# Performance work log

Hardware: AMD Instinct MI355X
Metric: run time of the kernel (lower is better)

The kernel has to match this reference:

```python
import jax, jax.numpy as jnp
import numpy as np

K = 10
EPS = 1e-5  # BatchNorm eps, eval mode with running_mean=0, running_var=1


def mish(x):
    return x * jnp.tanh(jax.nn.softplus(x))


def knn_idx(x, k):
    # x: (B, C, N); returns (B, N, k) indices of k nearest neighbors (incl. self)
    xx = jnp.sum(x * x, axis=1)                      # (B, N)
    inner = jnp.einsum('bcn,bcm->bnm', x, x)         # (B, N, N)
    neg_d = 2.0 * inner - xx[:, :, None] - xx[:, None, :]
    return jax.lax.top_k(neg_d, k)[1]


def graph_feature(x, k):
    # x: (B, C, N) -> edge features (B, 2C, N, k): cat(nbr - x, x)
    idx = knn_idx(x, k)
    x_t = jnp.transpose(x, (0, 2, 1))                # (B, N, C)
    nbr = jax.vmap(lambda xt, ix: xt[ix])(x_t, idx)  # (B, N, k, C)
    ctr = jnp.broadcast_to(x_t[:, :, None, :], nbr.shape)
    edge = jnp.concatenate([nbr - ctr, ctr], axis=-1)
    return jnp.transpose(edge, (0, 3, 1, 2))


def block2d(x, W, g, b):
    # Conv2d(kernel=1, bias=False) + BatchNorm2d(eval) + Mish
    y = jnp.einsum('oi,bink->bonk', W, x)
    y = y * (g / jnp.sqrt(1.0 + EPS))[None, :, None, None] + b[None, :, None, None]
    return mish(y)


def block1d(x, W, g, b):
    # Conv1d(kernel=1, bias=False) + BatchNorm1d(eval) + Mish
    y = jnp.einsum('oi,bin->bon', W, x)
    y = y * (g / jnp.sqrt(1.0 + EPS))[None, :, None] + b[None, :, None]
    return mish(y)


def setup_inputs() -> dict:
    key = jax.random.key(0)
    ks = jax.random.split(key, 32)
    B, N = 8, 4096
    x = jax.random.normal(ks[0], (B, 3, N), dtype=jnp.float32)

    def w(k, o, i):
        return jax.random.normal(k, (o, i), dtype=jnp.float32) * np.float32(np.sqrt(2.0 / i))

    W1 = w(ks[1], 64, 6)
    W2 = w(ks[2], 64, 128)
    W3 = w(ks[3], 128, 128)
    W4 = w(ks[4], 128, 128)
    W5 = w(ks[5], 128, 256)
    W6 = w(ks[6], 64, 128)
    W7 = w(ks[7], 64, 128)
    W8 = w(ks[8], 64, 128)
    W9 = w(ks[9], 2, 64)

    bn_sizes = [64, 64, 128, 128, 128, 64, 64, 64]
    gs, bs = [], []
    for i, c in enumerate(bn_sizes):
        gs.append(1.0 + 0.1 * jax.random.normal(ks[10 + i], (c,), dtype=jnp.float32))
        bs.append(0.1 * jax.random.normal(ks[20 + i], (c,), dtype=jnp.float32))

    d = {'x': x, 'W1': W1, 'W2': W2, 'W3': W3, 'W4': W4, 'W5': W5,
         'W6': W6, 'W7': W7, 'W8': W8, 'W9': W9}
    for i in range(8):
        d['g%d' % (i + 1)] = gs[i]
        d['b%d' % (i + 1)] = bs[i]
    return d


def reference(x, W1, W2, W3, W4, W5, W6, W7, W8, W9,
              g1, g2, g3, g4, g5, g6, g7, g8,
              b1, b2, b3, b4, b5, b6, b7, b8):
    e = graph_feature(x, K)                      # (B, 6, N, k)
    x1 = jnp.max(block2d(e, W1, g1, b1), axis=-1)  # (B, 64, N)
    e = graph_feature(x1, K)                     # (B, 128, N, k)
    x2 = jnp.max(block2d(e, W2, g2, b2), axis=-1)  # (B, 64, N)
    e = graph_feature(x2, K)                     # (B, 128, N, k)
    x3 = jnp.max(block2d(e, W3, g3, b3), axis=-1)  # (B, 128, N)
    h = block1d(x3, W4, g4, b4)                  # (B, 128, N)
    h = block1d(jnp.concatenate([h, x3], axis=1), W5, g5, b5)  # (B, 128, N)
    h = block1d(h, W6, g6, b6)                   # (B, 64, N)
    h = block1d(jnp.concatenate([h, x2], axis=1), W7, g7, b7)  # (B, 64, N)
    h = block1d(jnp.concatenate([h, x1], axis=1), W8, g8, b8)  # (B, 64, N)
    return jnp.einsum('oi,bin->bon', W9, h)      # (B, 2, N)
```

## Files before the change

### kernel.cpp

```cpp
#include <hip/hip_runtime.h>
#include <hip/hip_bf16.h>
#include <math.h>
#include <float.h>

#define B_ 8
#define N_ 4096
#define M_ (B_*N_)
#define KNN 10

typedef unsigned long long ull;
typedef __attribute__((ext_vector_type(8))) short s16x8;
typedef __attribute__((ext_vector_type(4))) float f32x4;

__device__ __forceinline__ float mishf(float x){
  float sp = (x > 20.f) ? x : __logf(1.f + __expf(x));
  float e2 = __expf(-2.f*sp);
  float th = (1.f - e2) / (1.f + e2);
  return x * th;
}

__device__ __forceinline__ ull shfl_xor_u64(ull v, int mask){
  unsigned lo = (unsigned)v, hi = (unsigned)(v >> 32);
  lo = (unsigned)__shfl_xor((int)lo, mask);
  hi = (unsigned)__shfl_xor((int)hi, mask);
  return ((ull)hi << 32) | lo;
}
__device__ __forceinline__ ull shfl_u64(ull v, int src){
  unsigned lo = (unsigned)v, hi = (unsigned)(v >> 32);
  lo = (unsigned)__shfl((int)lo, src);
  hi = (unsigned)__shfl((int)hi, src);
  return ((ull)hi << 32) | lo;
}
__device__ __forceinline__ int mbcnt_lt(ull mask){
  return __builtin_amdgcn_mbcnt_hi((unsigned)(mask>>32),
         __builtin_amdgcn_mbcnt_lo((unsigned)mask, 0));
}
__device__ __forceinline__ unsigned mono_u32(float f){
  unsigned u = __float_as_uint(f);
  return u ^ ((unsigned)((int)u >> 31) | 0x80000000u);
}
__device__ __forceinline__ float unmono(unsigned vk){
  unsigned u = (vk & 0x80000000u) ? (vk ^ 0x80000000u) : ~vk;
  return __uint_as_float(u);
}
__device__ __forceinline__ void gload_lds16(const void* g, void* l){
  __builtin_amdgcn_global_load_lds(
      (const __attribute__((address_space(1))) unsigned int*)g,
      (__attribute__((address_space(3))) unsigned int*)l, 16, 0, 0);
}

__global__ __launch_bounds__(256) void k_transpose_x(const float* __restrict__ x,
                                                     float* __restrict__ xp,
                                                     float4* __restrict__ xp4){
  int n = blockIdx.x*256 + threadIdx.x;
  if (n >= M_) return;
  int b = n >> 12, i = n & (N_-1);
  const float* xb = x + (size_t)b*3*N_;
  float v0 = xb[i], v1 = xb[N_+i], v2 = xb[2*N_+i];
  float* o = xp + (size_t)n*3;
  o[0]=v0; o[1]=v1; o[2]=v2;
  float s = fmaf(v0,v0,0.f); s = fmaf(v1,v1,s); s = fmaf(v2,v2,s);
  xp4[n] = make_float4(v0, v1, v2, -0.5f*s);
}

__global__ __launch_bounds__(256) void k_cvtxx(const float* __restrict__ X,
                                               ushort* __restrict__ Xhi,
                                               ushort* __restrict__ Xlo,
                                               float* __restrict__ xx){
  int n = blockIdx.x*256 + threadIdx.x;
  if (n >= M_) return;
  const float* r = X + (size_t)n*64;
  ushort* oh = Xhi + (size_t)n*64;
  ushort* ol = Xlo + (size_t)n*64;
  float s = 0.f;
#pragma unroll
  for (int g=0; g<8; ++g){
    float4 v0 = *(const float4*)(r + g*8);
    float4 v1 = *(const float4*)(r + g*8 + 4);
    float vv[8] = {v0.x,v0.y,v0.z,v0.w,v1.x,v1.y,v1.z,v1.w};
    unsigned hw[8], lw[8];
#pragma unroll
    for (int e=0;e<8;e++){
      float v = vv[e];
      s = fmaf(v,v,s);
      __hip_bfloat16 hb = __float2bfloat16(v);
      float hf = __bfloat162float(hb);
      __hip_bfloat16 lb = __float2bfloat16(v-hf);
      hw[e] = *(ushort*)&hb; lw[e] = *(ushort*)&lb;
    }
    uint4 hp, lp;
    hp.x = hw[0]|(hw[1]<<16); hp.y = hw[2]|(hw[3]<<16);
    hp.z = hw[4]|(hw[5]<<16); hp.w = hw[6]|(hw[7]<<16);
    lp.x = lw[0]|(lw[1]<<16); lp.y = lw[2]|(lw[3]<<16);
    lp.z = lw[4]|(lw[5]<<16); lp.w = lw[6]|(lw[7]<<16);
    *(uint4*)(oh + g*8) = hp;
    *(uint4*)(ol + g*8) = lp;
  }
  xx[n] = s;
}

__global__ __launch_bounds__(256) void k_knn3s(const float4* __restrict__ xp4,
                                               ull* __restrict__ part){
  const int bid   = blockIdx.x;
  const int piece = bid & 7;
  const int rg    = (bid >> 3) & 15;
  const int b     = bid >> 7;
  const int t     = threadIdx.x;
  const int row   = rg*256 + t;
  const float4 xi = xp4[(size_t)b*N_ + row];
  const float4* xj = xp4 + (size_t)b*N_ + piece*512;
  const int jbase = piece*512;

  ull kq[KNN];
#pragma unroll
  for (int q=0;q<KNN;q++) kq[q] = 0x007FFFFF00000000ull;
  float T = -INFINITY;

  for (int jc=0; jc<512; jc+=8){
    float4 c[8];
#pragma unroll
    for (int u=0;u<8;u++) c[u] = xj[jc+u];
#pragma unroll
    for (int u=0;u<8;u++){
      float a = fmaf(xi.x, c[u].x, 0.f);
      a = fmaf(xi.y, c[u].y, a);
      a = fmaf(xi.z, c[u].z, a);
      float v = a + c[u].w;
      if (v > T){
        unsigned jinv = 4095u - (unsigned)(jbase + jc + u);
        ull ck = ((ull)mono_u32(v)<<32) | jinv;
#pragma unroll
        for (int q=0;q<KNN;q++){
          ull hi = ck > kq[q] ? ck : kq[q];
          ull lo = ck > kq[q] ? kq[q] : ck;
          kq[q] = hi; ck = lo;
        }
        T = unmono((unsigned)(kq[KNN-1] >> 32));
      }
    }
  }

  ull* o = part + ((size_t)(b*N_ + row)*8 + piece)*KNN;
#pragma unroll
  for (int q=0;q<KNN;q++) o[q] = kq[q];
}

__global__ __launch_bounds__(256) void k_knnmerge8(const ull* __restrict__ part,
                                                   int* __restrict__ idxout){
  int row = blockIdx.x*256 + threadIdx.x;
  if (row >= M_) return;
  const ull* p = part + (size_t)row*8*KNN;
  unsigned P = 0;
  int* o = idxout + (size_t)row*KNN;
  for (int s=0;s<KNN;s++){
    ull best = 0; int bl = 0;
#pragma unroll
    for (int l=0;l<8;l++){
      unsigned pl = (P >> (4*l)) & 15u;
      ull k = p[l*KNN + pl];
      if (k > best){ best = k; bl = l; }
    }
    P += 1u << (4*bl);
    o[s] = (int)(4095u - ((unsigned)best & 4095u));
  }
}

__global__ __launch_bounds__(256,2) void k_knn64m(const ushort* __restrict__ Xhi,
                                                  const ushort* __restrict__ Xlo,
                                                  const float* __restrict__ xx,
                                                  int* __restrict__ idxout){
  constexpr int JT  = 128;
  constexpr int NT  = N_/JT;
  constexpr int CAP = 320;
  __shared__ ushort XJhi[2][JT*64];
  __shared__ ushort XJlo[2][JT*64];
  __shared__ float  halfxx[2][JT];
  __shared__ ull    buf[4][CAP];

  const int t    = threadIdx.x;
  const int w    = t >> 6;
  const int lane = t & 63;
  const int b    = blockIdx.x & 7;
  const int i0   = (blockIdx.x >> 3) * 64;
  const size_t rowbase = (size_t)b*N_;
  const float* xxb = xx + rowbase;

  const int arow = i0 + w*16 + (lane & 15);
  const ushort* Ah = Xhi + (rowbase + arow)*64;
  const ushort* Al = Xlo + (rowbase + arow)*64;
  const int ko = (lane >> 4)*8;
  s16x8 aH0 = *(const s16x8*)(Ah + ko);
  s16x8 aH1 = *(const s16x8*)(Ah + 32 + ko);
  s16x8 aL0 = *(const s16x8*)(Al + ko);
  s16x8 aL1 = *(const s16x8*)(Al + 32 + ko);

  ull kq[KNN];
#pragma unroll
  for (int q=0;q<KNN;q++) kq[q]=0ull;
  float Treg = -INFINITY;

  const int lr = lane >> 3;
  const int sc = (lane & 7) ^ lr;

  {
#pragma unroll
    for (int seg=0; seg<4; ++seg){
      const int row0 = w*32 + seg*8;
      gload_lds16(Xhi + (rowbase + row0 + lr)*64 + sc*8, &XJhi[0][row0*64]);
      gload_lds16(Xlo + (rowbase + row0 + lr)*64 + sc*8, &XJlo[0][row0*64]);
    }
    if (t < JT) halfxx[0][t] = 0.5f*xxb[t];
  }
  __syncthreads();

  for (int jt = 0; jt < NT; ++jt){
    const int cur = jt & 1;
    const int j0 = jt*JT;

    float hnext = 0.f;
    if (jt < NT-1){
      const size_t nb0 = rowbase + j0 + JT;
#pragma unroll
      for (int seg=0; seg<4; ++seg){
        const int row0 = w*32 + seg*8;
        gload_lds16(Xhi + (nb0 + row0 + lr)*64 + sc*8, &XJhi[cur^1][row0*64]);
        gload_lds16(Xlo + (nb0 + row0 + lr)*64 + sc*8, &XJlo[cur^1][row0*64]);
      }
      if (t < JT) hnext = 0.5f*xxb[j0 + JT + t];
    }

    f32x4 acc[8];
#pragma unroll
    for (int cb=0;cb<8;cb++) acc[cb] = (f32x4){0.f,0.f,0.f,0.f};

#pragma unroll
    for (int cb=0;cb<8;cb++){
      const int brow = cb*16 + (lane & 15);
      const unsigned sw = ((unsigned)(brow & 7)) << 4;
      const char* ph = (const char*)&XJhi[cur][0] + brow*128;
      const char* pl = (const char*)&XJlo[cur][0] + brow*128;
      const int kb0 = (int)((unsigned)((lane>>4)<<4) ^ sw);
      const int kb1 = (int)((unsigned)(64 | ((lane>>4)<<4)) ^ sw);
      s16x8 bh0 = *(const s16x8*)(ph + kb0);
      s16x8 bl0 = *(const s16x8*)(pl + kb0);
      s16x8 bh1 = *(const s16x8*)(ph + kb1);
      s16x8 bl1 = *(const s16x8*)(pl + kb1);
      f32x4 a = acc[cb];
      a = __builtin_amdgcn_mfma_f32_16x16x32_bf16(aH0, bh0, a, 0,0,0);
      a = __builtin_amdgcn_mfma_f32_16x16x32_bf16(aH0, bl0, a, 0,0,0);
      a = __builtin_amdgcn_mfma_f32_16x16x32_bf16(aL0, bh0, a, 0,0,0);
      a = __builtin_amdgcn_mfma_f32_16x16x32_bf16(aL0, bl0, a, 0,0,0);
      a = __builtin_amdgcn_mfma_f32_16x16x32_bf16(aH1, bh1, a, 0,0,0);
      a = __builtin_amdgcn_mfma_f32_16x16x32_bf16(aH1, bl1, a, 0,0,0);
      a = __builtin_amdgcn_mfma_f32_16x16x32_bf16(aL1, bh1, a, 0,0,0);
      a = __builtin_amdgcn_mfma_f32_16x16x32_bf16(aL1, bl1, a, 0,0,0);
      acc[cb] = a;
    }

    float hx[8];
#pragma unroll
    for (int cb=0;cb<8;cb++) hx[cb] = halfxx[cur][cb*16 + (lane & 15)];

    if (jt < NT-1 && t < JT) halfxx[cur^1][t] = hnext;

    if (jt == 0){
#pragma unroll
      for (int reg=0;reg<4;reg++){
        const unsigned rl = (unsigned)((lane>>4)*4 + reg);
        ull k8[8];
#pragma unroll
        for (int cb=0;cb<8;cb++){
          float v = acc[cb][reg] - hx[cb];
          unsigned jinv = 4095u - (unsigned)(cb*16 + (lane & 15));
          k8[cb] = ((ull)mono_u32(v)<<32) | ((ull)jinv<<4) | rl;
        }
#pragma unroll
        for (int q=0;q<KNN;q++){
          ull m = k8[0];
#pragma unroll
          for (int s=1;s<8;s++) m = m > k8[s] ? m : k8[s];
          ull v1 = shfl_xor_u64(m,1); m = m>v1?m:v1;
          ull v2 = shfl_xor_u64(m,2); m = m>v2?m:v2;
          ull v4 = shfl_xor_u64(m,4); m = m>v4?m:v4;
          ull v8 = shfl_xor_u64(m,8); m = m>v8?m:v8;
          ull mv = shfl_u64(m, (lane>>2)<<4);
          if (lane < 16 && (lane&3)==reg) kq[q] = mv;
#pragma unroll
          for (int s=0;s<8;s++) k8[s] = (k8[s]==m) ? 0ull : k8[s];
        }
      }
      Treg = unmono((unsigned)(kq[KNN-1] >> 32));
    } else {
      float Tf[4];
#pragma unroll
      for (int reg=0;reg<4;reg++) Tf[reg] = __shfl(Treg, (lane>>4)*4 + reg);
      int cnt = 0;
#pragma unroll
      for (int cb=0;cb<8;cb++){
#pragma unroll
        for (int reg=0;reg<4;reg++){
          float v = acc[cb][reg] - hx[cb];
          bool pass = v >= Tf[reg];
          ull mask = __ballot(pass);
          if (mask){
            if (pass){
              int slot = cnt + mbcnt_lt(mask);
              unsigned jinv = 4095u - (unsigned)(j0 + cb*16 + (lane & 15));
              ull key = ((ull)mono_u32(v)<<32) | ((ull)jinv<<4)
                        | (unsigned)((lane>>4)*4 + reg);
              if (slot < CAP) buf[w][slot] = key;
            }
            cnt += __popcll(mask);
          }
        }
      }
      if (cnt){
        int nb = cnt < CAP ? cnt : CAP;
        int pad = (4 - (nb & 3)) & 3;
        if (lane < pad && nb + lane < CAP) buf[w][nb + lane] = 0ull;
        int nb4 = nb + pad; if (nb4 > CAP) nb4 = CAP;
        for (int e=0;e<nb4;e+=4){
          ull c0=buf[w][e+0], c1=buf[w][e+1], c2=buf[w][e+2], c3=buf[w][e+3];
#pragma unroll
          for (int u=0;u<4;u++){
            ull k64 = (u==0)?c0:(u==1)?c1:(u==2)?c2:c3;
            if ((int)(k64 & 15ull) == lane && k64 > kq[KNN-1]){
              ull ck = k64;
#pragma unroll
              for (int q=0;q<KNN;q++){
                ull hi = ck > kq[q] ? ck : kq[q];
                ull lo = ck > kq[q] ? kq[q] : ck;
                kq[q] = hi; ck = lo;
              }
            }
          }
        }
        Treg = unmono((unsigned)(kq[KNN-1] >> 32));
      }
    }
    __syncthreads();
  }

  if (lane < 16){
    int* o = idxout + ((size_t)b*N_ + i0 + w*16 + lane)*KNN;
#pragma unroll
    for (int q=0;q<KNN;q++) o[q] = (int)(4095u - (unsigned)((kq[q]>>4) & 4095ull));
  }
}

template<int PT>
__global__ __launch_bounds__(256) void k_gemm(
    const float* __restrict__ X1, int C1,
    const float* __restrict__ X2, int C2,
    const float* __restrict__ W, int hmask, int hshift, int wstride, int hoff,
    const float* __restrict__ g, const float* __restrict__ bb, int act,
    float* __restrict__ Y, int Pfull)
{
  constexpr int CPT = PT/16;
  constexpr int WLS = PT + 4;
  __shared__ float Xt[32*68];
  __shared__ float Wt[32*WLS];
  const int t  = threadIdx.x;
  const int r0 = blockIdx.x*64;
  const int p0 = blockIdx.y*PT;
  const int cg = t & 15, rg = t >> 4;
  const int C = C1 + C2;
  const int nkt = (C + 31) >> 5;

  float acc[4][CPT];
#pragma unroll
  for (int a=0;a<4;a++)
#pragma unroll
    for (int c=0;c<CPT;c++) acc[a][c]=0.f;

  for (int kt = 0; kt < nkt; ++kt){
    const int k0 = kt*32;
#pragma unroll
    for (int e = t; e < 64*32; e += 256){
      int kk = e & 31, r = e >> 5;
      int gk = k0 + kk;
      float v = 0.f;
      if (gk < C1) v = X1[(size_t)(r0+r)*C1 + gk];
      else if (gk < C) v = X2[(size_t)(r0+r)*C2 + (gk - C1)];
      Xt[kk*68 + r] = v;
    }
#pragma unroll
    for (int e = t; e < PT*32; e += 256){
      int kk = e & 31, p = e >> 5;
      int gp = p0 + p;
      int wrow = (gp & hmask)*wstride + (gp >> hshift)*hoff;
      int gk = k0 + kk;
      Wt[kk*WLS + p] = (gk < C) ? W[(size_t)wrow + gk] : 0.f;
    }
    __syncthreads();
#pragma unroll
    for (int kk=0;kk<32;kk++){
      float4 xv = *(const float4*)&Xt[kk*68 + rg*4];
      float xr[4] = {xv.x, xv.y, xv.z, xv.w};
      float wv[CPT];
#pragma unroll
      for (int c4=0;c4<CPT/4;c4++){
        float4 w4 = *(const float4*)&Wt[kk*WLS + cg*CPT + c4*4];
        wv[c4*4+0]=w4.x; wv[c4*4+1]=w4.y; wv[c4*4+2]=w4.z; wv[c4*4+3]=w4.w;
      }
#pragma unroll
      for (int rr=0;rr<4;rr++)
#pragma unroll
        for (int cc=0;cc<CPT;cc++)
          acc[rr][cc] = fmaf(xr[rr], wv[cc], acc[rr][cc]);
    }
    __syncthreads();
  }

  const float srs = rsqrtf(1.f + 1e-5f);
  float sv[CPT], bvv[CPT];
#pragma unroll
  for (int cc=0;cc<CPT;cc++){
    int gp = p0 + cg*CPT + cc;
    if (g){ sv[cc] = g[gp]*srs; bvv[cc] = bb[gp]; } else { sv[cc]=1.f; bvv[cc]=0.f; }
  }
#pragma unroll
  for (int rr=0;rr<4;rr++){
    size_t row = r0 + rg*4 + rr;
    float* yr = Y + row*(size_t)Pfull + p0 + cg*CPT;
#pragma unroll
    for (int c4=0;c4<CPT/4;c4++){
      float y0 = sv[c4*4+0]*acc[rr][c4*4+0] + bvv[c4*4+0];
      float y1 = sv[c4*4+1]*acc[rr][c4*4+1] + bvv[c4*4+1];
      float y2 = sv[c4*4+2]*acc[rr][c4*4+2] + bvv[c4*4+2];
      float y3 = sv[c4*4+3]*acc[rr][c4*4+3] + bvv[c4*4+3];
      if (act){ y0=mishf(y0); y1=mishf(y1); y2=mishf(y2); y3=mishf(y3); }
      *(float4*)&yr[c4*4] = make_float4(y0,y1,y2,y3);
    }
  }
}

__global__ __launch_bounds__(256) void k_gemm8f(
    const float* __restrict__ X1, const float* __restrict__ X2,
    const float* __restrict__ W, const float* __restrict__ g,
    const float* __restrict__ bb, const float* __restrict__ W9,
    float* __restrict__ out)
{
  __shared__ float Xt[32*68];
  __shared__ float Wt[32*68];
  __shared__ float w9s[128];
  const int t  = threadIdx.x;
  const int r0 = blockIdx.x*64;
  const int cg = t & 15, rg = t >> 4;
  if (t < 128) w9s[t] = W9[t];

  float acc[4][4];
#pragma unroll
  for (int a=0;a<4;a++)
#pragma unroll
    for (int c=0;c<4;c++) acc[a][c]=0.f;

  for (int kt = 0; kt < 4; ++kt){
    const int k0 = kt*32;
#pragma unroll
    for (int e = t; e < 64*32; e += 256){
      int kk = e & 31, r = e >> 5;
      int gk = k0 + kk;
      float v = (gk < 64) ? X1[(size_t)(r0+r)*64 + gk]
                          : X2[(size_t)(r0+r)*64 + (gk - 64)];
      Xt[kk*68 + r] = v;
    }
#pragma unroll
    for (int e = t; e < 64*32; e += 256){
      int kk = e & 31, p = e >> 5;
      Wt[kk*68 + p] = W[(size_t)p*128 + k0 + kk];
    }
    __syncthreads();
#pragma unroll
    for (int kk=0;kk<32;kk++){
      float4 xv = *(const float4*)&Xt[kk*68 + rg*4];
      float xr[4] = {xv.x, xv.y, xv.z, xv.w};
      float4 w4 = *(const float4*)&Wt[kk*68 + cg*4];
      float wv[4] = {w4.x, w4.y, w4.z, w4.w};
#pragma unroll
      for (int rr=0;rr<4;rr++)
#pragma unroll
        for (int cc=0;cc<4;cc++)
          acc[rr][cc] = fmaf(xr[rr], wv[cc], acc[rr][cc]);
    }
    __syncthreads();
  }

  const float srs = rsqrtf(1.f + 1e-5f);
  float s0[4] = {0.f,0.f,0.f,0.f}, s1[4] = {0.f,0.f,0.f,0.f};
#pragma unroll
  for (int cc=0;cc<4;cc++){
    int p = cg*4 + cc;
    float sv = g[p]*srs, bv = bb[p];
    float w90 = w9s[p], w91 = w9s[64+p];
#pragma unroll
    for (int rr=0;rr<4;rr++){
      float y = mishf(fmaf(sv, acc[rr][cc], bv));
      s0[rr] = fmaf(w90, y, s0[rr]);
      s1[rr] = fmaf(w91, y, s1[rr]);
    }
  }
#pragma unroll
  for (int rr=0;rr<4;rr++){
    float v0 = s0[rr], v1 = s1[rr];
#pragma unroll
    for (int m=1;m<16;m<<=1){
      v0 += __shfl_xor(v0, m);
      v1 += __shfl_xor(v1, m);
    }
    if (cg == 0){
      int row = r0 + rg*4 + rr;
      int b = row >> 12, i = row & (N_-1);
      out[((size_t)b*2 + 0)*N_ + i] = v0;
      out[((size_t)b*2 + 1)*N_ + i] = v1;
    }
  }
}

template<int O>
__global__ __launch_bounds__(256) void k_edgemax(
    const float* __restrict__ ua, const int* __restrict__ idx,
    const float* __restrict__ g, const float* __restrict__ bb,
    float* __restrict__ Y)
{
  constexpr int TPR = O/4;
  const int gt = blockIdx.x*256 + threadIdx.x;
  const int m  = gt / TPR;
  const int og = gt % TPR;
  if (m >= M_) return;
  const int base = m & ~(N_-1);
  const int P = 2*O;
  const float4 u0 = *(const float4*)&ua[(size_t)m*P + og*4];
  const float4 a0 = *(const float4*)&ua[(size_t)m*P + O + og*4];
  const float srs = rsqrtf(1.f + 1e-5f);
  const float4 gv  = *(const float4*)&g[og*4];
  const float4 bv4 = *(const float4*)&bb[og*4];
  const float sx = gv.x*srs, sy = gv.y*srs, sz = gv.z*srs, sw = gv.w*srs;
  const float cx = a0.x - u0.x, cy = a0.y - u0.y, cz = a0.z - u0.z, cw = a0.w - u0.w;
  float mx = -INFINITY, my = -INFINITY, mz = -INFINITY, mw = -INFINITY;
  const int* id = idx + (size_t)m*KNN;
#pragma unroll
  for (int k=0;k<KNN;k++){
    int j = id[k];
    const float4 uj = *(const float4*)&ua[(size_t)(base + j)*P + og*4];
    float zx = fmaf(sx, uj.x + cx, bv4.x);
    float zy = fmaf(sy, uj.y + cy, bv4.y);
    float zz = fmaf(sz, uj.z + cz, bv4.z);
    float zw = fmaf(sw, uj.w + cw, bv4.w);
    mx = fmaxf(mx, mishf(zx));
    my = fmaxf(my, mishf(zy));
    mz = fmaxf(mz, mishf(zz));
    mw = fmaxf(mw, mishf(zw));
  }
  *(float4*)&Y[(size_t)m*O + og*4] = make_float4(mx,my,mz,mw);
}

extern "C" void kernel_launch(void* const* d_in, const int* in_sizes, int n_in,
                              void* d_out, int out_size, void* d_ws, size_t ws_size,
                              hipStream_t stream)
{
  const float* x  = (const float*)d_in[0];
  const float* W1 = (const float*)d_in[1];
  const float* W2 = (const float*)d_in[2];
  const float* W3 = (const float*)d_in[3];
  const float* W4 = (const float*)d_in[4];
  const float* W5 = (const float*)d_in[5];
  const float* W6 = (const float*)d_in[6];
  const float* W7 = (const float*)d_in[7];
  const float* W8 = (const float*)d_in[8];
  const float* W9 = (const float*)d_in[9];
  const float* g1 = (const float*)d_in[10]; const float* b1 = (const float*)d_in[11];
  const float* g2 = (const float*)d_in[12]; const float* b2 = (const float*)d_in[13];
  const float* g3 = (const float*)d_in[14]; const float* b3 = (const float*)d_in[15];
  const float* g4 = (const float*)d_in[16]; const float* b4 = (const float*)d_in[17];
  const float* g5 = (const float*)d_in[18]; const float* b5 = (const float*)d_in[19];
  const float* g6 = (const float*)d_in[20]; const float* b6 = (const float*)d_in[21];
  const float* g7 = (const float*)d_in[22]; const float* b7 = (const float*)d_in[23];
  const float* g8 = (const float*)d_in[24]; const float* b8 = (const float*)d_in[25];
  float* out = (float*)d_out;

  float* ws  = (float*)d_ws;
  float* xp  = ws;
  float* xx  = xp + 98304;
  float4* xp4 = (float4*)(xx + 32768);
  int*   idx = (int*)(xx + 32768 + 131072);
  float* ua  = (float*)(idx + 327680);
  float* x1  = ua + 8388608;
  float* x2  = x1 + 2097152;
  float* x3  = x2 + 2097152;
  float* h4  = x3 + 4194304;
  float* h5  = h4 + 4194304;
  float* h6  = x3;
  float* h7  = h4;
  ushort* Xhi = (ushort*)ua;
  ushort* Xlo = (ushort*)(ua + 1048576);
  ull*    part = (ull*)(ua + 2097152);

  const dim3 blk(256);
  const float* nullf = nullptr;

  k_transpose_x<<<dim3(M_/256), blk, 0, stream>>>(x, xp, xp4);
  k_knn3s<<<dim3(1024), blk, 0, stream>>>(xp4, part);
  k_knnmerge8<<<dim3(M_/256), blk, 0, stream>>>(part, idx);
  k_gemm<128><<<dim3(M_/64, 1), blk, 0, stream>>>(xp, 3, nullf, 0,
      W1, 63, 6, 6, 3, nullf, nullf, 0, ua, 128);
  k_edgemax<64><<<dim3(M_*16/256), blk, 0, stream>>>(ua, idx, g1, b1, x1);

  k_cvtxx<<<dim3(M_/256), blk, 0, stream>>>(x1, Xhi, Xlo, xx);
  k_knn64m<<<dim3(512), blk, 0, stream>>>(Xhi, Xlo, xx, idx);
  k_gemm<128><<<dim3(M_/64, 1), blk, 0, stream>>>(x1, 64, nullf, 0,
      W2, 63, 6, 128, 64, nullf, nullf, 0, ua, 128);
  k_edgemax<64><<<dim3(M_*16/256), blk, 0, stream>>>(ua, idx, g2, b2, x2);

  k_cvtxx<<<dim3(M_/256), blk, 0, stream>>>(x2, Xhi, Xlo, xx);
  k_knn64m<<<dim3(512), blk, 0, stream>>>(Xhi, Xlo, xx, idx);
  k_gemm<128><<<dim3(M_/64, 2), blk, 0, stream>>>(x2, 64, nullf, 0,
      W3, 127, 7, 128, 64, nullf, nullf, 0, ua, 256);
  k_edgemax<128><<<dim3(M_*32/256), blk, 0, stream>>>(ua, idx, g3, b3, x3);

  k_gemm<128><<<dim3(M_/64, 1), blk, 0, stream>>>(x3, 128, nullf, 0,
      W4, 127, 7, 128, 0, g4, b4, 1, h4, 128);
  k_gemm<128><<<dim3(M_/64, 1), blk, 0, stream>>>(h4, 128, x3, 128,
      W5, 127, 7, 256, 0, g5, b5, 1, h5, 128);
  k_gemm<64><<<dim3(M_/64, 1), blk, 0, stream>>>(h5, 128, nullf, 0,
      W6, 63, 6, 128, 0, g6, b6, 1, h6, 64);
  k_gemm<64><<<dim3(M_/64, 1), blk, 0, stream>>>(h6, 64, x2, 64,
      W7, 63, 6, 128, 0, g7, b7, 1, h7, 64);
  k_gemm8f<<<dim3(M_/64), blk, 0, stream>>>(h7, x1, W8, g8, b8, W9, out);
}
```

Before: 1.460 ms.

## Fuse point-wise MLP tail into two kernels keeping intermediates in LDS

Replaces the five separate per-layer GEMM launches (W4..W8+W9) with two fused kernels: one computes h4 into shared memory and feeds it straight into the W5 layer, and the other chains W6, W7 and W8+W9 through shared-memory tiles. This removes the global-memory writes and re-reads of the h4, h6 and h7 intermediates and three launches. In exchange each block uses much more LDS (about 50KB in k_mlp45), which lowers occupancy, and the GEMM inner loops remain scalar FP32 FMA.

```diff
diff --git a/kernel.cpp b/kernel.cpp
--- a/kernel.cpp
+++ b/kernel.cpp
@@ -435,67 +435,298 @@
   }
 }
 
-__global__ __launch_bounds__(256) void k_gemm8f(
-    const float* __restrict__ X1, const float* __restrict__ X2,
-    const float* __restrict__ W, const float* __restrict__ g,
-    const float* __restrict__ bb, const float* __restrict__ W9,
-    float* __restrict__ out)
+__global__ __launch_bounds__(256) void k_mlp45(
+    const float* __restrict__ x3g,
+    const float* __restrict__ W4, const float* __restrict__ g4, const float* __restrict__ b4,
+    const float* __restrict__ W5, const float* __restrict__ g5, const float* __restrict__ b5,
+    float* __restrict__ h5)
+{
+  __shared__ float Xt[32*68];
+  __shared__ float Wt[32*132];
+  __shared__ float h4t[64*132];
+  const int t  = threadIdx.x;
+  const int r0 = blockIdx.x*64;
+  const int cg = t & 15, rg = t >> 4;
+  const float srs = rsqrtf(1.f + 1e-5f);
+
+  {
+    float acc[4][8];
+#pragma unroll
+    for (int a=0;a<4;a++)
+#pragma unroll
+      for (int c=0;c<8;c++) acc[a][c]=0.f;
+    for (int kt = 0; kt < 4; ++kt){
+      const int k0 = kt*32;
+#pragma unroll
+      for (int e = t; e < 64*32; e += 256){
+        int kk = e & 31, r = e >> 5;
+        Xt[kk*68 + r] = x3g[(size_t)(r0+r)*128 + k0 + kk];
+      }
+#pragma unroll
+      for (int e = t; e < 128*32; e += 256){
+        int kk = e & 31, p = e >> 5;
+        Wt[kk*132 + p] = W4[(size_t)p*128 + k0 + kk];
+      }
+      __syncthreads();
+#pragma unroll
+      for (int kk=0;kk<32;kk++){
+        float4 xv = *(const float4*)&Xt[kk*68 + rg*4];
+        float xr[4] = {xv.x, xv.y, xv.z, xv.w};
+        float wv[8];
+#pragma unroll
+        for (int c4=0;c4<2;c4++){
+          float4 w4v = *(const float4*)&Wt[kk*132 + cg*8 + c4*4];
+          wv[c4*4+0]=w4v.x; wv[c4*4+1]=w4v.y; wv[c4*4+2]=w4v.z; wv[c4*4+3]=w4v.w;
+        }
+#pragma unroll
+        for (int rr=0;rr<4;rr++)
+#pragma unroll
+          for (int cc=0;cc<8;cc++)
+            acc[rr][cc] = fmaf(xr[rr], wv[cc], acc[rr][cc]);
+      }
+      __syncthreads();
+    }
+    float sv[8], bvv[8];
+#pragma unroll
+    for (int cc=0;cc<8;cc++){
+      int gp = cg*8 + cc;
+      sv[cc] = g4[gp]*srs; bvv[cc] = b4[gp];
+    }
+#pragma unroll
+    for (int rr=0;rr<4;rr++){
+      int row = rg*4 + rr;
+#pragma unroll
+      for (int cc=0;cc<8;cc++){
+        float y = sv[cc]*acc[rr][cc] + bvv[cc];
+        h4t[row*132 + cg*8 + cc] = mishf(y);
+      }
+    }
+  }
+  __syncthreads();
+
+  {
+    float acc[4][8];
+#pragma unroll
+    for (int a=0;a<4;a++)
+#pragma unroll
+      for (int c=0;c<8;c++) acc[a][c]=0.f;
+    for (int kt = 0; kt < 8; ++kt){
+      const int k0 = kt*32;
+#pragma unroll
+      for (int e = t; e < 64*32; e += 256){
+        int kk = e & 31, r = e >> 5;
+        int gk = k0 + kk;
+        float v = (gk < 128) ? h4t[r*132 + gk]
+                             : x3g[(size_t)(r0+r)*128 + (gk - 128)];
+        Xt[kk*68 + r] = v;
+      }
+#pragma unroll
+      for (int e = t; e < 128*32; e += 256){
+        int kk = e & 31, p = e >> 5;
+        Wt[kk*132 + p] = W5[(size_t)p*256 + k0 + kk];
+      }
+      __syncthreads();
+#pragma unroll
+      for (int kk=0;kk<32;kk++){
+        float4 xv = *(const float4*)&Xt[kk*68 + rg*4];
+        float xr[4] = {xv.x, xv.y, xv.z, xv.w};
+        float wv[8];
+#pragma unroll
+        for (int c4=0;c4<2;c4++){
+          float4 w4v = *(const float4*)&Wt[kk*132 + cg*8 + c4*4];
+          wv[c4*4+0]=w4v.x; wv[c4*4+1]=w4v.y; wv[c4*4+2]=w4v.z; wv[c4*4+3]=w4v.w;
+        }
+#pragma unroll
+        for (int rr=0;rr<4;rr++)
+#pragma unroll
+          for (int cc=0;cc<8;cc++)
+            acc[rr][cc] = fmaf(xr[rr], wv[cc], acc[rr][cc]);
+      }
+      __syncthreads();
+    }
+    float sv[8], bvv[8];
+#pragma unroll
+    for (int cc=0;cc<8;cc++){
+      int gp = cg*8 + cc;
+      sv[cc] = g5[gp]*srs; bvv[cc] = b5[gp];
+    }
+#pragma unroll
+    for (int rr=0;rr<4;rr++){
+      size_t row = r0 + rg*4 + rr;
+      float* yr = h5 + row*128 + cg*8;
+#pragma unroll
+      for (int c4=0;c4<2;c4++){
+        float y0 = sv[c4*4+0]*acc[rr][c4*4+0] + bvv[c4*4+0];
+        float y1 = sv[c4*4+1]*acc[rr][c4*4+1] + bvv[c4*4+1];
+        float y2 = sv[c4*4+2]*acc[rr][c4*4+2] + bvv[c4*4+2];
+        float y3 = sv[c4*4+3]*acc[rr][c4*4+3] + bvv[c4*4+3];
+        *(float4*)&yr[c4*4] = make_float4(mishf(y0),mishf(y1),mishf(y2),mishf(y3));
+      }
+    }
+  }
+}
+
+__global__ __launch_bounds__(256) void k_mlp69(
+    const float* __restrict__ h5g, const float* __restrict__ x2g, const float* __restrict__ x1g,
+    const float* __restrict__ W6, const float* __restrict__ g6, const float* __restrict__ b6,
+    const float* __restrict__ W7, const float* __restrict__ g7, const float* __restrict__ b7,
+    const float* __restrict__ W8, const float* __restrict__ g8, const float* __restrict__ b8,
+    const float* __restrict__ W9, float* __restrict__ out)
 {
   __shared__ float Xt[32*68];
   __shared__ float Wt[32*68];
+  __shared__ float h6t[64*68];
+  __shared__ float h7t[64*68];
   __shared__ float w9s[128];
   const int t  = threadIdx.x;
   const int r0 = blockIdx.x*64;
   const int cg = t & 15, rg = t >> 4;
+  const float srs = rsqrtf(1.f + 1e-5f);
   if (t < 128) w9s[t] = W9[t];
 
-  float acc[4][4];
-#pragma unroll
-  for (int a=0;a<4;a++)
-#pragma unroll
-    for (int c=0;c<4;c++) acc[a][c]=0.f;
-
-  for (int kt = 0; kt < 4; ++kt){
-    const int k0 = kt*32;
-#pragma unroll
-    for (int e = t; e < 64*32; e += 256){
-      int kk = e & 31, r = e >> 5;
-      int gk = k0 + kk;
-      float v = (gk < 64) ? X1[(size_t)(r0+r)*64 + gk]
-                          : X2[(size_t)(r0+r)*64 + (gk - 64)];
-      Xt[kk*68 + r] = v;
-    }
-#pragma unroll
-    for (int e = t; e < 64*32; e += 256){
-      int kk = e & 31, p = e >> 5;
-      Wt[kk*68 + p] = W[(size_t)p*128 + k0 + kk];
-    }
-    __syncthreads();
-#pragma unroll
-    for (int kk=0;kk<32;kk++){
-      float4 xv = *(const float4*)&Xt[kk*68 + rg*4];
-      float xr[4] = {xv.x, xv.y, xv.z, xv.w};
-      float4 w4 = *(const float4*)&Wt[kk*68 + cg*4];
-      float wv[4] = {w4.x, w4.y, w4.z, w4.w};
-#pragma unroll
-      for (int rr=0;rr<4;rr++)
-#pragma unroll
-        for (int cc=0;cc<4;cc++)
-          acc[rr][cc] = fmaf(xr[rr], wv[cc], acc[rr][cc]);
-    }
-    __syncthreads();
-  }
-
-  const float srs = rsqrtf(1.f + 1e-5f);
+  float acc8[4][4];
+
+  {
+    float acc[4][4];
+#pragma unroll
+    for (int a=0;a<4;a++)
+#pragma unroll
+      for (int c=0;c<4;c++) acc[a][c]=0.f;
+    for (int kt = 0; kt < 4; ++kt){
+      const int k0 = kt*32;
+#pragma unroll
+      for (int e = t; e < 64*32; e += 256){
+        int kk = e & 31, r = e >> 5;
+        Xt[kk*68 + r] = h5g[(size_t)(r0+r)*128 + k0 + kk];
+      }
+#pragma unroll
+      for (int e = t; e < 64*32; e += 256){
+        int kk = e & 31, p = e >> 5;
+        Wt[kk*68 + p] = W6[(size_t)p*128 + k0 + kk];
+      }
+      __syncthreads();
+#pragma unroll
+      for (int kk=0;kk<32;kk++){
+        float4 xv = *(const float4*)&Xt[kk*68 + rg*4];
+        float xr[4] = {xv.x, xv.y, xv.z, xv.w};
+        float4 w4v = *(const float4*)&Wt[kk*68 + cg*4];
+        float wv[4] = {w4v.x, w4v.y, w4v.z, w4v.w};
+#pragma unroll
+        for (int rr=0;rr<4;rr++)
+#pragma unroll
+          for (int cc=0;cc<4;cc++)
+            acc[rr][cc] = fmaf(xr[rr], wv[cc], acc[rr][cc]);
+      }
+      __syncthreads();
+    }
+#pragma unroll
+    for (int cc=0;cc<4;cc++){
+      int gp = cg*4 + cc;
+      float sv = g6[gp]*srs, bv = b6[gp];
+#pragma unroll
+      for (int rr=0;rr<4;rr++){
+        float y = sv*acc[rr][cc] + bv;
+        h6t[(rg*4+rr)*68 + gp] = mishf(y);
+      }
+    }
+  }
+  __syncthreads();
+
+  {
+    float acc[4][4];
+#pragma unroll
+    for (int a=0;a<4;a++)
+#pragma unroll
+      for (int c=0;c<4;c++) acc[a][c]=0.f;
+    for (int kt = 0; kt < 4; ++kt){
+      const int k0 = kt*32;
+#pragma unroll
+      for (int e = t; e < 64*32; e += 256){
+        int kk = e & 31, r = e >> 5;
+        int gk = k0 + kk;
+        float v = (gk < 64) ? h6t[r*68 + gk]
+                            : x2g[(size_t)(r0+r)*64 + (gk - 64)];
+        Xt[kk*68 + r] = v;
+      }
+#pragma unroll
+      for (int e = t; e < 64*32; e += 256){
+        int kk = e & 31, p = e >> 5;
+        Wt[kk*68 + p] = W7[(size_t)p*128 + k0 + kk];
+      }
+      __syncthreads();
+#pragma unroll
+      for (int kk=0;kk<32;kk++){
+        float4 xv = *(const float4*)&Xt[kk*68 + rg*4];
+        float xr[4] = {xv.x, xv.y, xv.z, xv.w};
+        float4 w4v = *(const float4*)&Wt[kk*68 + cg*4];
+        float wv[4] = {w4v.x, w4v.y, w4v.z, w4v.w};
+#pragma unroll
+        for (int rr=0;rr<4;rr++)
+#pragma unroll
+          for (int cc=0;cc<4;cc++)
+            acc[rr][cc] = fmaf(xr[rr], wv[cc], acc[rr][cc]);
+      }
+      __syncthreads();
+    }
+#pragma unroll
+    for (int cc=0;cc<4;cc++){
+      int gp = cg*4 + cc;
+      float sv = g7[gp]*srs, bv = b7[gp];
+#pragma unroll
+      for (int rr=0;rr<4;rr++){
+        float y = sv*acc[rr][cc] + bv;
+        h7t[(rg*4+rr)*68 + gp] = mishf(y);
+      }
+    }
+  }
+  __syncthreads();
+
+  {
+#pragma unroll
+    for (int a=0;a<4;a++)
+#pragma unroll
+      for (int c=0;c<4;c++) acc8[a][c]=0.f;
+    for (int kt = 0; kt < 4; ++kt){
+      const int k0 = kt*32;
+#pragma unroll
+      for (int e = t; e < 64*32; e += 256){
+        int kk = e & 31, r = e >> 5;
+        int gk = k0 + kk;
+        float v = (gk < 64) ? h7t[r*68 + gk]
+                            : x1g[(size_t)(r0+r)*64 + (gk - 64)];
+        Xt[kk*68 + r] = v;
+      }
+#pragma unroll
+      for (int e = t; e < 64*32; e += 256){
+        int kk = e & 31, p = e >> 5;
+        Wt[kk*68 + p] = W8[(size_t)p*128 + k0 + kk];
+      }
+      __syncthreads();
+#pragma unroll
+      for (int kk=0;kk<32;kk++){
+        float4 xv = *(const float4*)&Xt[kk*68 + rg*4];
+        float xr[4] = {xv.x, xv.y, xv.z, xv.w};
+        float4 w4v = *(const float4*)&Wt[kk*68 + cg*4];
+        float wv[4] = {w4v.x, w4v.y, w4v.z, w4v.w};
+#pragma unroll
+        for (int rr=0;rr<4;rr++)
+#pragma unroll
+          for (int cc=0;cc<4;cc++)
+            acc8[rr][cc] = fmaf(xr[rr], wv[cc], acc8[rr][cc]);
+      }
+      __syncthreads();
+    }
+  }
+
   float s0[4] = {0.f,0.f,0.f,0.f}, s1[4] = {0.f,0.f,0.f,0.f};
 #pragma unroll
   for (int cc=0;cc<4;cc++){
     int p = cg*4 + cc;
-    float sv = g[p]*srs, bv = bb[p];
+    float sv = g8[p]*srs, bv = b8[p];
     float w90 = w9s[p], w91 = w9s[64+p];
 #pragma unroll
     for (int rr=0;rr<4;rr++){
-      float y = mishf(fmaf(sv, acc[rr][cc], bv));
+      float y = mishf(fmaf(sv, acc8[rr][cc], bv));
       s0[rr] = fmaf(w90, y, s0[rr]);
       s1[rr] = fmaf(w91, y, s1[rr]);
     }
@@ -588,10 +819,7 @@
   float* x1  = ua + 8388608;
   float* x2  = x1 + 2097152;
   float* x3  = x2 + 2097152;
-  float* h4  = x3 + 4194304;
-  float* h5  = h4 + 4194304;
-  float* h6  = x3;
-  float* h7  = h4;
+  float* h5  = x3 + 4194304;
   ushort* Xhi = (ushort*)ua;
   ushort* Xlo = (ushort*)(ua + 1048576);
   ull*    part = (ull*)(ua + 2097152);
@@ -618,13 +846,7 @@
       W3, 127, 7, 128, 64, nullf, nullf, 0, ua, 256);
   k_edgemax<128><<<dim3(M_*32/256), blk, 0, stream>>>(ua, idx, g3, b3, x3);
 
-  k_gemm<128><<<dim3(M_/64, 1), blk, 0, stream>>>(x3, 128, nullf, 0,
-      W4, 127, 7, 128, 0, g4, b4, 1, h4, 128);
-  k_gemm<128><<<dim3(M_/64, 1), blk, 0, stream>>>(h4, 128, x3, 128,
-      W5, 127, 7, 256, 0, g5, b5, 1, h5, 128);
-  k_gemm<64><<<dim3(M_/64, 1), blk, 0, stream>>>(h5, 128, nullf, 0,
-      W6, 63, 6, 128, 0, g6, b6, 1, h6, 64);
-  k_gemm<64><<<dim3(M_/64, 1), blk, 0, stream>>>(h6, 64, x2, 64,
-      W7, 63, 6, 128, 0, g7, b7, 1, h7, 64);
-  k_gemm8f<<<dim3(M_/64), blk, 0, stream>>>(h7, x1, W8, g8, b8, W9, out);
-}
+  k_mlp45<<<dim3(M_/64), blk, 0, stream>>>(x3, W4, g4, b4, W5, g5, b5, h5);
+  k_mlp69<<<dim3(M_/64), blk, 0, stream>>>(h5, x2, x1,
+      W6, g6, b6, W7, g7, b7, W8, g8, b8, W9, out);
+}
```

Measured after the change: 1.484 ms. No clear change (+1.7%).
